# Optimization experiments

Measured on AMD Instinct MI355X. Metric: run time of the kernel, lower is better.

Reference implementation:

```python
import math
import jax, jax.numpy as jnp
import numpy as np

_GELU_C = math.sqrt(2.0 / math.pi)

def _gelu_tanh(x):
    return 0.5 * x * (1.0 + jnp.tanh(_GELU_C * (x + 0.044715 * x * x * x)))

def _l2_normalize(v, eps=1e-12):
    # matches F.normalize: v / max(||v||, eps)
    n = jnp.sqrt(jnp.sum(v * v, axis=-1, keepdims=True))
    return v / jnp.maximum(n, eps)

def setup_inputs() -> dict:
    key = jax.random.key(0)
    k1, k2, k3 = jax.random.split(key, 3)
    B, T, D = 8, 2048, 1024
    x = jax.random.normal(k1, (B, T, D), dtype=jnp.float32)
    # nn.Parameter initial values from the module
    log_alpha = jnp.asarray(math.log(math.exp(0.5) - 1.0), dtype=jnp.float32)
    log_sigma = jnp.asarray(math.log(1.0), dtype=jnp.float32)
    return {"x": x, "log_alpha": log_alpha, "log_sigma": log_sigma}

def reference(x, log_alpha, log_sigma):
    B, T, D = x.shape
    alpha = jax.nn.softplus(log_alpha)
    sigma = jax.nn.softplus(log_sigma)
    scale = 1.0 / math.sqrt(D)
    # full strictly-past causal attention (triu with diagonal=0 masks self too)
    sim = jnp.einsum('btd,bsd->bts', x, x) * scale            # [B,T,T]
    causal = jnp.triu(jnp.ones((T, T), dtype=bool), k=0)      # True = masked
    sim = jnp.where(causal[None], -jnp.inf, sim)
    # NaN-safe masked softmax: fully-masked rows (t=0) -> all zeros,
    # matching torch softmax + nan_to_num(nan=0.0)
    m = jnp.max(sim, axis=-1, keepdims=True)
    m_safe = jnp.where(jnp.isfinite(m), m, 0.0)
    e = jnp.exp(sim - m_safe)                                 # -inf -> 0
    denom = jnp.sum(e, axis=-1, keepdims=True)
    attn = jnp.where(denom > 0, e / jnp.where(denom > 0, denom, 1.0), 0.0)
    context = jnp.einsum('bts,bsd->btd', attn, x)             # [B,T,D]
    cos_sim = jnp.sum(_l2_normalize(x) * _l2_normalize(context), axis=-1)  # [B,T]
    novelty = jnp.clip(1.0 - cos_sim, 0.0, 2.0) / 2.0
    novelty = jnp.nan_to_num(novelty, nan=1.0)
    gate = 1.0 + alpha * jnp.tanh(sigma * novelty[..., None])
    return _gelu_tanh(x * gate)
```

## Files before the change

### kernel.cpp

```cpp
#include <hip/hip_runtime.h>
#include <math.h>

#define TN 2048
#define DN 1024
#define NEG_INF (-3.0e38f)

typedef __attribute__((ext_vector_type(8))) _Float16 half8;
typedef __attribute__((ext_vector_type(4))) _Float16 half4v;
typedef __attribute__((ext_vector_type(4))) float f32x4;

__device__ __forceinline__ f32x4 mfma16(half8 a, half8 b, f32x4 c) {
  return __builtin_amdgcn_mfma_f32_16x16x32_f16(a, b, c, 0, 0, 0);
}

#define BAR_LDS() asm volatile("s_waitcnt lgkmcnt(0)\ns_barrier" ::: "memory")

__device__ __forceinline__ int img_off(int key, int f) {
  const int kg = key >> 2;
  const int p  = ((kg & 1) << 2) | (kg >> 1);
  return (f >> 4) * 512 + p * 64 + (key & 3) * 16 + (f & 15);
}

__global__ __launch_bounds__(256) void convert_x(const float* __restrict__ x,
                                                 _Float16* __restrict__ w) {
  const long long gid = (long long)blockIdx.x * 256 + threadIdx.x;
  const long long e   = gid * 8;
  const int bt   = (int)(e >> 15);
  const int et   = (int)(e & 32767);
  const int f16b = et >> 9;
  const int p    = (et >> 6) & 7;
  const int row  = (et >> 4) & 3;
  const int col0 = et & 15;
  const int kg   = ((p & 3) << 1) | (p >> 2);
  const int key  = kg * 4 + row;
  const size_t xoff = ((size_t)bt * 32 + key) * DN + f16b * 16 + col0;
  float4 u0 = *(const float4*)(x + xoff);
  float4 u1 = *(const float4*)(x + xoff + 4);
  half8 h = {(_Float16)u0.x, (_Float16)u0.y, (_Float16)u0.z, (_Float16)u0.w,
             (_Float16)u1.x, (_Float16)u1.y, (_Float16)u1.z, (_Float16)u1.w};
  *(half8*)(w + e) = h;
}

template <bool WS>
__global__ __launch_bounds__(512)
void attn_gate(const float* __restrict__ x, const _Float16* __restrict__ wsx,
               const float* __restrict__ pla, const float* __restrict__ pls,
               float* __restrict__ out) {
  __shared__ _Float16 Kbuf[2][32768];
  __shared__ float Sred[4][32][34];
  __shared__ _Float16 Pq[32][40];
  __shared__ float m_s[32], l_s[32], corr_s[32], gate_s[32];

  const int tid = threadIdx.x;
  const int w   = tid >> 6;
  const int l   = tid & 63;
  const int lr  = l & 15;
  const int lg  = l >> 4;
  const int kq  = w & 3;
  const int ti  = w >> 2;

  const int b  = blockIdx.x & 7;
  const int pr = blockIdx.x >> 3;

  const float alpha = log1pf(expf(pla[0]));
  const float sigma = log1pf(expf(pls[0]));

  const float* xb = x + (size_t)b * TN * DN;
  float*       ob = out + (size_t)b * TN * DN;

  for (int hv = 0; hv < 2; ++hv) {
    const int qt    = hv ? (63 - pr) : pr;
    const int qbase = qt * 32;
    const int nkt   = qt + 1;

    if constexpr (WS) {
      const _Float16* t0 = wsx + (size_t)(b * 64 + 0) * 32768;
#pragma unroll
      for (int i = 0; i < 8; ++i)
        __builtin_amdgcn_global_load_lds(
            (const __attribute__((address_space(1))) void*)(t0 + w * 4096 + i * 512 + l * 8),
            (__attribute__((address_space(3))) void*)(&Kbuf[0][w * 4096 + i * 512]), 16, 0, 0);
      if (nkt > 1) {
        const _Float16* t1 = wsx + (size_t)(b * 64 + 1) * 32768;
#pragma unroll
        for (int i = 0; i < 8; ++i)
          __builtin_amdgcn_global_load_lds(
              (const __attribute__((address_space(1))) void*)(t1 + w * 4096 + i * 512 + l * 8),
              (__attribute__((address_space(3))) void*)(&Kbuf[1][w * 4096 + i * 512]), 16, 0, 0);
      }
    } else {
      const int skey = tid >> 4, sc = tid & 15;
      for (int t = 0; t < (nkt > 1 ? 2 : 1); ++t) {
        const float* kp = xb + (size_t)(t * 32 + skey) * DN + sc * 4;
#pragma unroll
        for (int j = 0; j < 16; ++j) {
          const int f = sc * 4 + 64 * j;
          float4 v = *(const float4*)(kp + 64 * j);
          half4v h = {(_Float16)v.x, (_Float16)v.y, (_Float16)v.z, (_Float16)v.w};
          *(half4v*)&Kbuf[t][img_off(skey, f)] = h;
        }
      }
    }

    half8 qf[8];
    if constexpr (WS) {
      const _Float16* qtile = wsx + (size_t)(b * 64 + qt) * 32768;
      const int qrow = ti * 16 + lr;
      const int qkg  = qrow >> 2;
      const int qp   = (((qkg & 1) << 2) | (qkg >> 1)) * 64 + (qrow & 3) * 16 + (lg & 1) * 8;
#pragma unroll
      for (int s = 0; s < 8; ++s)
        qf[s] = *(const half8*)&qtile[(kq * 16 + s * 2 + (lg >> 1)) * 512 + qp];
    } else {
      const float* qp = xb + (size_t)(qbase + ti * 16 + lr) * DN + kq * 256 + lg * 8;
#pragma unroll
      for (int s = 0; s < 8; ++s) {
        float4 a = ((const float4*)(qp + s * 32))[0];
        float4 c = ((const float4*)(qp + s * 32))[1];
        half8 h;
        h[0]=(_Float16)a.x; h[1]=(_Float16)a.y; h[2]=(_Float16)a.z; h[3]=(_Float16)a.w;
        h[4]=(_Float16)c.x; h[5]=(_Float16)c.y; h[6]=(_Float16)c.z; h[7]=(_Float16)c.w;
        qf[s] = h;
      }
    }

    f32x4 oacc[2][8];
#pragma unroll
    for (int rt = 0; rt < 2; ++rt)
#pragma unroll
      for (int ct = 0; ct < 8; ++ct)
        oacc[rt][ct] = f32x4{0.f, 0.f, 0.f, 0.f};

    if (tid < 32) { m_s[tid] = NEG_INF; l_s[tid] = 0.0f; }
    __syncthreads();

    const int kg0  = lr >> 2;
    const int bk0  = ((((kg0 & 1) << 2) | (kg0 >> 1)) << 6) + (lr & 3) * 16 + (lg & 1) * 8;
    const int kg1  = 4 + (lr >> 2);
    const int bk1  = ((((kg1 & 1) << 2) | (kg1 >> 1)) << 6) + (lr & 3) * 16 + (lg & 1) * 8;

    for (int kt = 0; kt < nkt; ++kt) {
      const int cur = kt & 1;

      {
        f32x4 s0 = f32x4{0.f, 0.f, 0.f, 0.f};
        f32x4 s1 = f32x4{0.f, 0.f, 0.f, 0.f};
        const _Float16* kb = &Kbuf[cur][0];
#pragma unroll
        for (int s = 0; s < 8; ++s) {
          const int base = (kq * 16 + s * 2 + (lg >> 1)) * 512;
          half8 bf0 = *(const half8*)&kb[base + bk0];
          half8 bf1 = *(const half8*)&kb[base + bk1];
          s0 = mfma16(qf[s], bf0, s0);
          s1 = mfma16(qf[s], bf1, s1);
        }
#pragma unroll
        for (int j = 0; j < 4; ++j) {
          Sred[kq][ti * 16 + lg * 4 + j][lr]      = s0[j];
          Sred[kq][ti * 16 + lg * 4 + j][16 + lr] = s1[j];
        }
      }
      BAR_LDS();

      {
        const int r   = tid >> 4;
        const int c0  = tid & 15;
        const int qg  = qbase + r;
        const int kb0 = kt * 32;
        float s0 = (Sred[0][r][c0] + Sred[1][r][c0] +
                    Sred[2][r][c0] + Sred[3][r][c0]) * 0.03125f;
        float s1 = (Sred[0][r][c0 + 16] + Sred[1][r][c0 + 16] +
                    Sred[2][r][c0 + 16] + Sred[3][r][c0 + 16]) * 0.03125f;
        const bool v0 = (kb0 + c0)      < qg;
        const bool v1 = (kb0 + c0 + 16) < qg;
        if (!v0) s0 = NEG_INF;
        if (!v1) s1 = NEG_INF;
        float tmax = fmaxf(s0, s1);
#pragma unroll
        for (int d = 1; d < 16; d <<= 1) tmax = fmaxf(tmax, __shfl_xor(tmax, d));
        const float m_old = m_s[r];
        const float m_new = fmaxf(m_old, tmax);
        float p0 = v0 ? __expf(s0 - m_new) : 0.0f;
        float p1 = v1 ? __expf(s1 - m_new) : 0.0f;
        float ps = p0 + p1;
#pragma unroll
        for (int d = 1; d < 16; d <<= 1) ps += __shfl_xor(ps, d);
        const float corr = (m_old > 0.5f * NEG_INF) ? __expf(m_old - m_new) : 0.0f;
        if (c0 == 0) {
          m_s[r]    = m_new;
          l_s[r]    = l_s[r] * corr + ps;
          corr_s[r] = corr;
        }
        Pq[r][c0]      = (_Float16)p0;
        Pq[r][c0 + 16] = (_Float16)p1;
      }
      BAR_LDS();

      {
#pragma unroll
        for (int rt = 0; rt < 2; ++rt)
#pragma unroll
          for (int j = 0; j < 4; ++j) {
            const float cr = corr_s[rt * 16 + lg * 4 + j];
#pragma unroll
            for (int ct = 0; ct < 8; ++ct) oacc[rt][ct][j] *= cr;
          }
        half8 a0 = *(const half8*)&Pq[lr][lg * 8];
        half8 a1 = *(const half8*)&Pq[16 + lr][lg * 8];
        half4v lo[8], hi[8];
        const uint32_t ab =
            (uint32_t)(uintptr_t)(void*)&Kbuf[cur][w * 4096 + l * 4];
#define TRRD(CT, O0, O1)                                                      \
        asm volatile("ds_read_b64_tr_b16 %0, %2 offset:" O0 "\n\t"            \
                     "ds_read_b64_tr_b16 %1, %2 offset:" O1                   \
                     : "=v"(lo[CT]), "=v"(hi[CT]) : "v"(ab));
        TRRD(0, "0",    "512")  TRRD(1, "1024", "1536")
        TRRD(2, "2048", "2560") TRRD(3, "3072", "3584")
        TRRD(4, "4096", "4608") TRRD(5, "5120", "5632")
        TRRD(6, "6144", "6656") TRRD(7, "7168", "7680")
#undef TRRD
        asm volatile("s_waitcnt lgkmcnt(0)" ::: "memory");
        __builtin_amdgcn_sched_barrier(0);
#pragma unroll
        for (int ct = 0; ct < 8; ++ct) {
          half8 bf = __builtin_shufflevector(lo[ct], hi[ct], 0, 1, 2, 3, 4, 5, 6, 7);
          oacc[0][ct] = mfma16(a0, bf, oacc[0][ct]);
          oacc[1][ct] = mfma16(a1, bf, oacc[1][ct]);
        }
      }
      __syncthreads();

      if (kt + 2 < nkt) {
        if constexpr (WS) {
          const _Float16* tn = wsx + (size_t)(b * 64 + kt + 2) * 32768;
#pragma unroll
          for (int i = 0; i < 8; ++i)
            __builtin_amdgcn_global_load_lds(
                (const __attribute__((address_space(1))) void*)(tn + w * 4096 + i * 512 + l * 8),
                (__attribute__((address_space(3))) void*)(&Kbuf[cur][w * 4096 + i * 512]), 16, 0, 0);
        } else {
          const int skey = tid >> 4, sc = tid & 15;
          const float* kp = xb + (size_t)((kt + 2) * 32 + skey) * DN + sc * 4;
#pragma unroll
          for (int j = 0; j < 16; ++j) {
            const int f = sc * 4 + 64 * j;
            float4 v = *(const float4*)(kp + 64 * j);
            half4v h = {(_Float16)v.x, (_Float16)v.y, (_Float16)v.z, (_Float16)v.w};
            *(half4v*)&Kbuf[cur][img_off(skey, f)] = h;
          }
        }
      }
    }

    {
      float* ered = &Sred[0][0][0];
#pragma unroll
      for (int rt = 0; rt < 2; ++rt)
#pragma unroll
        for (int j = 0; j < 4; ++j) {
          const int row = rt * 16 + lg * 4 + j;
          const float* xr = xb + (size_t)(qbase + row) * DN + w * 128 + lr;
          float a1 = 0.f, a2 = 0.f, a3 = 0.f;
#pragma unroll
          for (int ct = 0; ct < 8; ++ct) {
            const float xv = xr[ct * 16];
            const float ov = oacc[rt][ct][j];
            a1 += xv * ov; a2 += xv * xv; a3 += ov * ov;
          }
#pragma unroll
          for (int d = 1; d < 16; d <<= 1) {
            a1 += __shfl_xor(a1, d);
            a2 += __shfl_xor(a2, d);
            a3 += __shfl_xor(a3, d);
          }
          if (lr == 0) {
            float* e = ered + (row * 8 + w) * 4;
            e[0] = a1; e[1] = a2; e[2] = a3;
          }
        }
    }
    __syncthreads();
    if (tid < 32) {
      const float* ered = &Sred[0][0][0];
      float SxO = 0.f, Sxx = 0.f, SOO = 0.f;
#pragma unroll
      for (int wv = 0; wv < 8; ++wv) {
        const float* e = ered + (tid * 8 + wv) * 4;
        SxO += e[0]; Sxx += e[1]; SOO += e[2];
      }
      const float lden = l_s[tid];
      float cosv = 0.0f;
      if (lden > 0.0f) {
        const float nx = fmaxf(sqrtf(Sxx), 1e-12f);
        const float nc = fmaxf(sqrtf(SOO) / lden, 1e-12f);
        cosv = (SxO / lden) / (nx * nc);
      }
      float nov = fminf(fmaxf(1.0f - cosv, 0.0f), 2.0f) * 0.5f;
      gate_s[tid] = 1.0f + alpha * tanhf(sigma * nov);
    }
    __syncthreads();
    {
#pragma unroll
      for (int rt = 0; rt < 2; ++rt)
#pragma unroll
        for (int j = 0; j < 4; ++j) {
          const int row = rt * 16 + lg * 4 + j;
          const float g = gate_s[row];
          const float* xr = xb + (size_t)(qbase + row) * DN + w * 128 + lr;
          float* orow     = ob + (size_t)(qbase + row) * DN + w * 128 + lr;
#pragma unroll
          for (int ct = 0; ct < 8; ++ct) {
            const float z = xr[ct * 16] * g;
            const float u = 0.7978845608028654f * (z + 0.044715f * z * z * z);
            orow[ct * 16] = 0.5f * z * (1.0f + tanhf(u));
          }
        }
    }
    __syncthreads();
  }
}

extern "C" void kernel_launch(void* const* d_in, const int* in_sizes, int n_in,
                              void* d_out, int out_size, void* d_ws, size_t ws_size,
                              hipStream_t stream) {
  const float* x  = (const float*)d_in[0];
  const float* la = (const float*)d_in[1];
  const float* ls = (const float*)d_in[2];
  float* out = (float*)d_out;
  const size_t need = (size_t)8 * 64 * 32768 * 2;
  if (ws_size >= need) {
    convert_x<<<dim3(8192), dim3(256), 0, stream>>>(x, (_Float16*)d_ws);
    attn_gate<true><<<dim3(256), dim3(512), 0, stream>>>(
        x, (const _Float16*)d_ws, la, ls, out);
  } else {
    attn_gate<false><<<dim3(256), dim3(512), 0, stream>>>(
        x, (const _Float16*)nullptr, la, ls, out);
  }
}
```

Before: 196.5 us.

## Single-buffer K tile, one query tile per block, raise occupancy to 4 blocks/CU

Each block now handles one query tile (heaviest first) instead of a paired light/heavy tile, and the grid doubles to 512 blocks. The K tile drops from double to single buffering, and the score-reduction scratch is stored as fp16, shrinking LDS so that launch bounds of 4 blocks per CU can hold. The P·V step now interleaves transposed LDS reads with MFMAs and skips the accumulator rescale when no row max changed. The aim is latency hiding through more concurrent blocks rather than in-block prefetch, at the cost of an exposed load per key tile, less balanced per-block work, and fp16 rounding of partial scores.

```diff
diff --git a/kernel.cpp b/kernel.cpp
--- a/kernel.cpp
+++ b/kernel.cpp
@@ -7,13 +7,15 @@
 
 typedef __attribute__((ext_vector_type(8))) _Float16 half8;
 typedef __attribute__((ext_vector_type(4))) _Float16 half4v;
+typedef __attribute__((ext_vector_type(2))) _Float16 half2v;
 typedef __attribute__((ext_vector_type(4))) float f32x4;
 
 __device__ __forceinline__ f32x4 mfma16(half8 a, half8 b, f32x4 c) {
   return __builtin_amdgcn_mfma_f32_16x16x32_f16(a, b, c, 0, 0, 0);
 }
 
-#define BAR_LDS() asm volatile("s_waitcnt lgkmcnt(0)\ns_barrier" ::: "memory")
+#define BAR_LDS()  asm volatile("s_waitcnt lgkmcnt(0)\ns_barrier" ::: "memory")
+#define BAR_ALL()  asm volatile("s_waitcnt vmcnt(0) lgkmcnt(0)\ns_barrier" ::: "memory")
 
 __device__ __forceinline__ int img_off(int key, int f) {
   const int kg = key >> 2;
@@ -41,15 +43,34 @@
   *(half8*)(w + e) = h;
 }
 
+#define ISSUE4(T, O0, O1, O2, O3)                                             \
+  asm volatile("ds_read_b64_tr_b16 %0, %4 offset:" O0 "\n\t"                  \
+               "ds_read_b64_tr_b16 %1, %4 offset:" O1 "\n\t"                  \
+               "ds_read_b64_tr_b16 %2, %4 offset:" O2 "\n\t"                  \
+               "ds_read_b64_tr_b16 %3, %4 offset:" O3                         \
+               : "=&v"(T[0]), "=&v"(T[1]), "=&v"(T[2]), "=&v"(T[3])           \
+               : "v"(ab));
+
+#define MFMA4(T, CT0, CT1)                                                    \
+  {                                                                           \
+    half8 bf0 = __builtin_shufflevector(T[0], T[1], 0, 1, 2, 3, 4, 5, 6, 7);  \
+    half8 bf1 = __builtin_shufflevector(T[2], T[3], 0, 1, 2, 3, 4, 5, 6, 7);  \
+    oacc[0][CT0] = mfma16(a0, bf0, oacc[0][CT0]);                             \
+    oacc[1][CT0] = mfma16(a1, bf0, oacc[1][CT0]);                             \
+    oacc[0][CT1] = mfma16(a0, bf1, oacc[0][CT1]);                             \
+    oacc[1][CT1] = mfma16(a1, bf1, oacc[1][CT1]);                             \
+  }
+
 template <bool WS>
-__global__ __launch_bounds__(512)
+__global__ __launch_bounds__(512, 4)
 void attn_gate(const float* __restrict__ x, const _Float16* __restrict__ wsx,
                const float* __restrict__ pla, const float* __restrict__ pls,
                float* __restrict__ out) {
-  __shared__ _Float16 Kbuf[2][32768];
-  __shared__ float Sred[4][32][34];
+  __shared__ _Float16 Kbuf[32768];
+  __shared__ _Float16 SredH[4][32][17][2];
   __shared__ _Float16 Pq[32][40];
   __shared__ float m_s[32], l_s[32], corr_s[32], gate_s[32];
+  __shared__ int resc_s;
 
   const int tid = threadIdx.x;
   const int w   = tid >> 6;
@@ -60,7 +81,9 @@
   const int ti  = w >> 2;
 
   const int b  = blockIdx.x & 7;
-  const int pr = blockIdx.x >> 3;
+  const int qt = 63 - (blockIdx.x >> 3);
+  const int qbase = qt * 32;
+  const int nkt   = qt + 1;
 
   const float alpha = log1pf(expf(pla[0]));
   const float sigma = log1pf(expf(pls[0]));
@@ -68,255 +91,251 @@
   const float* xb = x + (size_t)b * TN * DN;
   float*       ob = out + (size_t)b * TN * DN;
 
-  for (int hv = 0; hv < 2; ++hv) {
-    const int qt    = hv ? (63 - pr) : pr;
-    const int qbase = qt * 32;
-    const int nkt   = qt + 1;
-
-    if constexpr (WS) {
-      const _Float16* t0 = wsx + (size_t)(b * 64 + 0) * 32768;
-#pragma unroll
-      for (int i = 0; i < 8; ++i)
-        __builtin_amdgcn_global_load_lds(
-            (const __attribute__((address_space(1))) void*)(t0 + w * 4096 + i * 512 + l * 8),
-            (__attribute__((address_space(3))) void*)(&Kbuf[0][w * 4096 + i * 512]), 16, 0, 0);
-      if (nkt > 1) {
-        const _Float16* t1 = wsx + (size_t)(b * 64 + 1) * 32768;
+  if constexpr (WS) {
+    const _Float16* t0 = wsx + (size_t)(b * 64 + 0) * 32768;
+#pragma unroll
+    for (int i = 0; i < 8; ++i)
+      __builtin_amdgcn_global_load_lds(
+          (const __attribute__((address_space(1))) void*)(t0 + w * 4096 + i * 512 + l * 8),
+          (__attribute__((address_space(3))) void*)(&Kbuf[w * 4096 + i * 512]), 16, 0, 0);
+  } else {
+    const int skey = tid >> 4, sc = tid & 15;
+    const float* kp = xb + (size_t)skey * DN + sc * 4;
+#pragma unroll
+    for (int j = 0; j < 16; ++j) {
+      const int f = sc * 4 + 64 * j;
+      float4 v = *(const float4*)(kp + 64 * j);
+      half4v h = {(_Float16)v.x, (_Float16)v.y, (_Float16)v.z, (_Float16)v.w};
+      *(half4v*)&Kbuf[img_off(skey, f)] = h;
+    }
+  }
+
+  half8 qf[8];
+  if constexpr (WS) {
+    const _Float16* qtile = wsx + (size_t)(b * 64 + qt) * 32768;
+    const int qrow = ti * 16 + lr;
+    const int qkg  = qrow >> 2;
+    const int qp   = (((qkg & 1) << 2) | (qkg >> 1)) * 64 + (qrow & 3) * 16 + (lg & 1) * 8;
+#pragma unroll
+    for (int s = 0; s < 8; ++s)
+      qf[s] = *(const half8*)&qtile[(kq * 16 + s * 2 + (lg >> 1)) * 512 + qp];
+  } else {
+    const float* qp = xb + (size_t)(qbase + ti * 16 + lr) * DN + kq * 256 + lg * 8;
+#pragma unroll
+    for (int s = 0; s < 8; ++s) {
+      float4 a = ((const float4*)(qp + s * 32))[0];
+      float4 c = ((const float4*)(qp + s * 32))[1];
+      half8 h;
+      h[0]=(_Float16)a.x; h[1]=(_Float16)a.y; h[2]=(_Float16)a.z; h[3]=(_Float16)a.w;
+      h[4]=(_Float16)c.x; h[5]=(_Float16)c.y; h[6]=(_Float16)c.z; h[7]=(_Float16)c.w;
+      qf[s] = h;
+    }
+  }
+
+  f32x4 oacc[2][8];
+#pragma unroll
+  for (int rt = 0; rt < 2; ++rt)
+#pragma unroll
+    for (int ct = 0; ct < 8; ++ct)
+      oacc[rt][ct] = f32x4{0.f, 0.f, 0.f, 0.f};
+
+  if (tid < 32) { m_s[tid] = NEG_INF; l_s[tid] = 0.0f; }
+  if (tid == 0) resc_s = 0;
+  BAR_ALL();
+
+  const int kg0 = lr >> 2;
+  const int bk0 = ((((kg0 & 1) << 2) | (kg0 >> 1)) << 6) + (lr & 3) * 16 + (lg & 1) * 8;
+  const int kg1 = 4 + (lr >> 2);
+  const int bk1 = ((((kg1 & 1) << 2) | (kg1 >> 1)) << 6) + (lr & 3) * 16 + (lg & 1) * 8;
+
+  for (int kt = 0; kt < nkt; ++kt) {
+    if (tid == 0) resc_s = 0;
+
+    {
+      f32x4 s0 = f32x4{0.f, 0.f, 0.f, 0.f};
+      f32x4 s1 = f32x4{0.f, 0.f, 0.f, 0.f};
+#pragma unroll
+      for (int s = 0; s < 8; ++s) {
+        const int base = (kq * 16 + s * 2 + (lg >> 1)) * 512;
+        half8 bf0 = *(const half8*)&Kbuf[base + bk0];
+        half8 bf1 = *(const half8*)&Kbuf[base + bk1];
+        s0 = mfma16(qf[s], bf0, s0);
+        s1 = mfma16(qf[s], bf1, s1);
+      }
+#pragma unroll
+      for (int j = 0; j < 4; ++j) {
+        half2v pr2 = {(_Float16)s0[j], (_Float16)s1[j]};
+        *(half2v*)&SredH[kq][ti * 16 + lg * 4 + j][lr][0] = pr2;
+      }
+    }
+    BAR_LDS();
+
+    {
+      const int r   = tid >> 4;
+      const int c0  = tid & 15;
+      const int qg  = qbase + r;
+      const int kb0 = kt * 32;
+      float s0 = 0.f, s1 = 0.f;
+#pragma unroll
+      for (int k4 = 0; k4 < 4; ++k4) {
+        half2v v = *(const half2v*)&SredH[k4][r][c0][0];
+        s0 += (float)v[0];
+        s1 += (float)v[1];
+      }
+      s0 *= 0.03125f; s1 *= 0.03125f;
+      const bool v0 = (kb0 + c0)      < qg;
+      const bool v1 = (kb0 + c0 + 16) < qg;
+      if (!v0) s0 = NEG_INF;
+      if (!v1) s1 = NEG_INF;
+      float tmax = fmaxf(s0, s1);
+#pragma unroll
+      for (int d = 1; d < 16; d <<= 1) tmax = fmaxf(tmax, __shfl_xor(tmax, d));
+      const float m_old = m_s[r];
+      const float m_new = fmaxf(m_old, tmax);
+      float p0 = v0 ? __expf(s0 - m_new) : 0.0f;
+      float p1 = v1 ? __expf(s1 - m_new) : 0.0f;
+      float ps = p0 + p1;
+#pragma unroll
+      for (int d = 1; d < 16; d <<= 1) ps += __shfl_xor(ps, d);
+      if (c0 == 0) {
+        const float corr = (m_old > 0.5f * NEG_INF) ? __expf(m_old - m_new) : 0.0f;
+        m_s[r]    = m_new;
+        l_s[r]    = l_s[r] * corr + ps;
+        corr_s[r] = corr;
+        if (m_new > m_old) resc_s = 1;
+      }
+      Pq[r][c0]      = (_Float16)p0;
+      Pq[r][c0 + 16] = (_Float16)p1;
+    }
+    BAR_LDS();
+
+    {
+      const int doresc = resc_s;
+      if (doresc) {
+#pragma unroll
+        for (int rt = 0; rt < 2; ++rt)
+#pragma unroll
+          for (int j = 0; j < 4; ++j) {
+            const float cr2 = corr_s[rt * 16 + lg * 4 + j];
+#pragma unroll
+            for (int ct = 0; ct < 8; ++ct) oacc[rt][ct][j] *= cr2;
+          }
+      }
+      const uint32_t pa0 = (uint32_t)(uintptr_t)(void*)&Pq[lr][lg * 8];
+      const uint32_t pa1 = (uint32_t)(uintptr_t)(void*)&Pq[16 + lr][lg * 8];
+      const uint32_t ab  = (uint32_t)(uintptr_t)(void*)&Kbuf[w * 4096 + l * 4];
+      asm volatile("s_waitcnt lgkmcnt(0)" ::: "memory");
+      __builtin_amdgcn_sched_barrier(0);
+      half8 a0, a1;
+      half4v t0[4], t1[4];
+      asm volatile("ds_read_b128 %0, %2\n\t"
+                   "ds_read_b128 %1, %3"
+                   : "=&v"(a0), "=&v"(a1) : "v"(pa0), "v"(pa1));
+      ISSUE4(t0, "0", "512", "1024", "1536");
+      ISSUE4(t1, "2048", "2560", "3072", "3584");
+      asm volatile("s_waitcnt lgkmcnt(4)" ::: "memory");
+      __builtin_amdgcn_sched_barrier(0);
+      MFMA4(t0, 0, 1);
+      ISSUE4(t0, "4096", "4608", "5120", "5632");
+      asm volatile("s_waitcnt lgkmcnt(4)" ::: "memory");
+      __builtin_amdgcn_sched_barrier(0);
+      MFMA4(t1, 2, 3);
+      ISSUE4(t1, "6144", "6656", "7168", "7680");
+      asm volatile("s_waitcnt lgkmcnt(4)" ::: "memory");
+      __builtin_amdgcn_sched_barrier(0);
+      MFMA4(t0, 4, 5);
+      asm volatile("s_waitcnt lgkmcnt(0)" ::: "memory");
+      __builtin_amdgcn_sched_barrier(0);
+      MFMA4(t1, 6, 7);
+    }
+    BAR_LDS();
+
+    if (kt + 1 < nkt) {
+      if constexpr (WS) {
+        const _Float16* tn = wsx + (size_t)(b * 64 + kt + 1) * 32768;
 #pragma unroll
         for (int i = 0; i < 8; ++i)
           __builtin_amdgcn_global_load_lds(
-              (const __attribute__((address_space(1))) void*)(t1 + w * 4096 + i * 512 + l * 8),
-              (__attribute__((address_space(3))) void*)(&Kbuf[1][w * 4096 + i * 512]), 16, 0, 0);
-      }
-    } else {
-      const int skey = tid >> 4, sc = tid & 15;
-      for (int t = 0; t < (nkt > 1 ? 2 : 1); ++t) {
-        const float* kp = xb + (size_t)(t * 32 + skey) * DN + sc * 4;
+              (const __attribute__((address_space(1))) void*)(tn + w * 4096 + i * 512 + l * 8),
+              (__attribute__((address_space(3))) void*)(&Kbuf[w * 4096 + i * 512]), 16, 0, 0);
+      } else {
+        const int skey = tid >> 4, sc = tid & 15;
+        const float* kp = xb + (size_t)((kt + 1) * 32 + skey) * DN + sc * 4;
 #pragma unroll
         for (int j = 0; j < 16; ++j) {
           const int f = sc * 4 + 64 * j;
           float4 v = *(const float4*)(kp + 64 * j);
           half4v h = {(_Float16)v.x, (_Float16)v.y, (_Float16)v.z, (_Float16)v.w};
-          *(half4v*)&Kbuf[t][img_off(skey, f)] = h;
-        }
-      }
-    }
-
-    half8 qf[8];
-    if constexpr (WS) {
-      const _Float16* qtile = wsx + (size_t)(b * 64 + qt) * 32768;
-      const int qrow = ti * 16 + lr;
-      const int qkg  = qrow >> 2;
-      const int qp   = (((qkg & 1) << 2) | (qkg >> 1)) * 64 + (qrow & 3) * 16 + (lg & 1) * 8;
-#pragma unroll
-      for (int s = 0; s < 8; ++s)
-        qf[s] = *(const half8*)&qtile[(kq * 16 + s * 2 + (lg >> 1)) * 512 + qp];
-    } else {
-      const float* qp = xb + (size_t)(qbase + ti * 16 + lr) * DN + kq * 256 + lg * 8;
-#pragma unroll
-      for (int s = 0; s < 8; ++s) {
-        float4 a = ((const float4*)(qp + s * 32))[0];
-        float4 c = ((const float4*)(qp + s * 32))[1];
-        half8 h;
-        h[0]=(_Float16)a.x; h[1]=(_Float16)a.y; h[2]=(_Float16)a.z; h[3]=(_Float16)a.w;
-        h[4]=(_Float16)c.x; h[5]=(_Float16)c.y; h[6]=(_Float16)c.z; h[7]=(_Float16)c.w;
-        qf[s] = h;
-      }
-    }
-
-    f32x4 oacc[2][8];
+          *(half4v*)&Kbuf[img_off(skey, f)] = h;
+        }
+      }
+      BAR_ALL();
+    }
+  }
+
+  {
+    float* ered = (float*)&SredH[0][0][0][0];
 #pragma unroll
     for (int rt = 0; rt < 2; ++rt)
 #pragma unroll
-      for (int ct = 0; ct < 8; ++ct)
-        oacc[rt][ct] = f32x4{0.f, 0.f, 0.f, 0.f};
-
-    if (tid < 32) { m_s[tid] = NEG_INF; l_s[tid] = 0.0f; }
-    __syncthreads();
-
-    const int kg0  = lr >> 2;
-    const int bk0  = ((((kg0 & 1) << 2) | (kg0 >> 1)) << 6) + (lr & 3) * 16 + (lg & 1) * 8;
-    const int kg1  = 4 + (lr >> 2);
-    const int bk1  = ((((kg1 & 1) << 2) | (kg1 >> 1)) << 6) + (lr & 3) * 16 + (lg & 1) * 8;
-
-    for (int kt = 0; kt < nkt; ++kt) {
-      const int cur = kt & 1;
-
-      {
-        f32x4 s0 = f32x4{0.f, 0.f, 0.f, 0.f};
-        f32x4 s1 = f32x4{0.f, 0.f, 0.f, 0.f};
-        const _Float16* kb = &Kbuf[cur][0];
-#pragma unroll
-        for (int s = 0; s < 8; ++s) {
-          const int base = (kq * 16 + s * 2 + (lg >> 1)) * 512;
-          half8 bf0 = *(const half8*)&kb[base + bk0];
-          half8 bf1 = *(const half8*)&kb[base + bk1];
-          s0 = mfma16(qf[s], bf0, s0);
-          s1 = mfma16(qf[s], bf1, s1);
-        }
-#pragma unroll
-        for (int j = 0; j < 4; ++j) {
-          Sred[kq][ti * 16 + lg * 4 + j][lr]      = s0[j];
-          Sred[kq][ti * 16 + lg * 4 + j][16 + lr] = s1[j];
-        }
-      }
-      BAR_LDS();
-
-      {
-        const int r   = tid >> 4;
-        const int c0  = tid & 15;
-        const int qg  = qbase + r;
-        const int kb0 = kt * 32;
-        float s0 = (Sred[0][r][c0] + Sred[1][r][c0] +
-                    Sred[2][r][c0] + Sred[3][r][c0]) * 0.03125f;
-        float s1 = (Sred[0][r][c0 + 16] + Sred[1][r][c0 + 16] +
-                    Sred[2][r][c0 + 16] + Sred[3][r][c0 + 16]) * 0.03125f;
-        const bool v0 = (kb0 + c0)      < qg;
-        const bool v1 = (kb0 + c0 + 16) < qg;
-        if (!v0) s0 = NEG_INF;
-        if (!v1) s1 = NEG_INF;
-        float tmax = fmaxf(s0, s1);
-#pragma unroll
-        for (int d = 1; d < 16; d <<= 1) tmax = fmaxf(tmax, __shfl_xor(tmax, d));
-        const float m_old = m_s[r];
-        const float m_new = fmaxf(m_old, tmax);
-        float p0 = v0 ? __expf(s0 - m_new) : 0.0f;
-        float p1 = v1 ? __expf(s1 - m_new) : 0.0f;
-        float ps = p0 + p1;
-#pragma unroll
-        for (int d = 1; d < 16; d <<= 1) ps += __shfl_xor(ps, d);
-        const float corr = (m_old > 0.5f * NEG_INF) ? __expf(m_old - m_new) : 0.0f;
-        if (c0 == 0) {
-          m_s[r]    = m_new;
-          l_s[r]    = l_s[r] * corr + ps;
-          corr_s[r] = corr;
-        }
-        Pq[r][c0]      = (_Float16)p0;
-        Pq[r][c0 + 16] = (_Float16)p1;
-      }
-      BAR_LDS();
-
-      {
-#pragma unroll
-        for (int rt = 0; rt < 2; ++rt)
-#pragma unroll
-          for (int j = 0; j < 4; ++j) {
-            const float cr = corr_s[rt * 16 + lg * 4 + j];
-#pragma unroll
-            for (int ct = 0; ct < 8; ++ct) oacc[rt][ct][j] *= cr;
-          }
-        half8 a0 = *(const half8*)&Pq[lr][lg * 8];
-        half8 a1 = *(const half8*)&Pq[16 + lr][lg * 8];
-        half4v lo[8], hi[8];
-        const uint32_t ab =
-            (uint32_t)(uintptr_t)(void*)&Kbuf[cur][w * 4096 + l * 4];
-#define TRRD(CT, O0, O1)                                                      \
-        asm volatile("ds_read_b64_tr_b16 %0, %2 offset:" O0 "\n\t"            \
-                     "ds_read_b64_tr_b16 %1, %2 offset:" O1                   \
-                     : "=v"(lo[CT]), "=v"(hi[CT]) : "v"(ab));
-        TRRD(0, "0",    "512")  TRRD(1, "1024", "1536")
-        TRRD(2, "2048", "2560") TRRD(3, "3072", "3584")
-        TRRD(4, "4096", "4608") TRRD(5, "5120", "5632")
-        TRRD(6, "6144", "6656") TRRD(7, "7168", "7680")
-#undef TRRD
-        asm volatile("s_waitcnt lgkmcnt(0)" ::: "memory");
-        __builtin_amdgcn_sched_barrier(0);
+      for (int j = 0; j < 4; ++j) {
+        const int row = rt * 16 + lg * 4 + j;
+        const float* xr = xb + (size_t)(qbase + row) * DN + w * 128 + lr;
+        float a1 = 0.f, a2 = 0.f, a3 = 0.f;
 #pragma unroll
         for (int ct = 0; ct < 8; ++ct) {
-          half8 bf = __builtin_shufflevector(lo[ct], hi[ct], 0, 1, 2, 3, 4, 5, 6, 7);
-          oacc[0][ct] = mfma16(a0, bf, oacc[0][ct]);
-          oacc[1][ct] = mfma16(a1, bf, oacc[1][ct]);
-        }
-      }
-      __syncthreads();
-
-      if (kt + 2 < nkt) {
-        if constexpr (WS) {
-          const _Float16* tn = wsx + (size_t)(b * 64 + kt + 2) * 32768;
-#pragma unroll
-          for (int i = 0; i < 8; ++i)
-            __builtin_amdgcn_global_load_lds(
-                (const __attribute__((address_space(1))) void*)(tn + w * 4096 + i * 512 + l * 8),
-                (__attribute__((address_space(3))) void*)(&Kbuf[cur][w * 4096 + i * 512]), 16, 0, 0);
-        } else {
-          const int skey = tid >> 4, sc = tid & 15;
-          const float* kp = xb + (size_t)((kt + 2) * 32 + skey) * DN + sc * 4;
-#pragma unroll
-          for (int j = 0; j < 16; ++j) {
-            const int f = sc * 4 + 64 * j;
-            float4 v = *(const float4*)(kp + 64 * j);
-            half4v h = {(_Float16)v.x, (_Float16)v.y, (_Float16)v.z, (_Float16)v.w};
-            *(half4v*)&Kbuf[cur][img_off(skey, f)] = h;
-          }
-        }
-      }
-    }
-
-    {
-      float* ered = &Sred[0][0][0];
-#pragma unroll
-      for (int rt = 0; rt < 2; ++rt)
-#pragma unroll
-        for (int j = 0; j < 4; ++j) {
-          const int row = rt * 16 + lg * 4 + j;
-          const float* xr = xb + (size_t)(qbase + row) * DN + w * 128 + lr;
-          float a1 = 0.f, a2 = 0.f, a3 = 0.f;
-#pragma unroll
-          for (int ct = 0; ct < 8; ++ct) {
-            const float xv = xr[ct * 16];
-            const float ov = oacc[rt][ct][j];
-            a1 += xv * ov; a2 += xv * xv; a3 += ov * ov;
-          }
-#pragma unroll
-          for (int d = 1; d < 16; d <<= 1) {
-            a1 += __shfl_xor(a1, d);
-            a2 += __shfl_xor(a2, d);
-            a3 += __shfl_xor(a3, d);
-          }
-          if (lr == 0) {
-            float* e = ered + (row * 8 + w) * 4;
-            e[0] = a1; e[1] = a2; e[2] = a3;
-          }
-        }
-    }
-    __syncthreads();
-    if (tid < 32) {
-      const float* ered = &Sred[0][0][0];
-      float SxO = 0.f, Sxx = 0.f, SOO = 0.f;
-#pragma unroll
-      for (int wv = 0; wv < 8; ++wv) {
-        const float* e = ered + (tid * 8 + wv) * 4;
-        SxO += e[0]; Sxx += e[1]; SOO += e[2];
-      }
-      const float lden = l_s[tid];
-      float cosv = 0.0f;
-      if (lden > 0.0f) {
-        const float nx = fmaxf(sqrtf(Sxx), 1e-12f);
-        const float nc = fmaxf(sqrtf(SOO) / lden, 1e-12f);
-        cosv = (SxO / lden) / (nx * nc);
-      }
-      float nov = fminf(fmaxf(1.0f - cosv, 0.0f), 2.0f) * 0.5f;
-      gate_s[tid] = 1.0f + alpha * tanhf(sigma * nov);
-    }
-    __syncthreads();
-    {
-#pragma unroll
-      for (int rt = 0; rt < 2; ++rt)
-#pragma unroll
-        for (int j = 0; j < 4; ++j) {
-          const int row = rt * 16 + lg * 4 + j;
-          const float g = gate_s[row];
-          const float* xr = xb + (size_t)(qbase + row) * DN + w * 128 + lr;
-          float* orow     = ob + (size_t)(qbase + row) * DN + w * 128 + lr;
-#pragma unroll
-          for (int ct = 0; ct < 8; ++ct) {
-            const float z = xr[ct * 16] * g;
-            const float u = 0.7978845608028654f * (z + 0.044715f * z * z * z);
-            orow[ct * 16] = 0.5f * z * (1.0f + tanhf(u));
-          }
-        }
-    }
-    __syncthreads();
+          const float xv = xr[ct * 16];
+          const float ov = oacc[rt][ct][j];
+          a1 += xv * ov; a2 += xv * xv; a3 += ov * ov;
+        }
+#pragma unroll
+        for (int d = 1; d < 16; d <<= 1) {
+          a1 += __shfl_xor(a1, d);
+          a2 += __shfl_xor(a2, d);
+          a3 += __shfl_xor(a3, d);
+        }
+        if (lr == 0) {
+          float* e = ered + (row * 8 + w) * 4;
+          e[0] = a1; e[1] = a2; e[2] = a3;
+        }
+      }
+  }
+  __syncthreads();
+  if (tid < 32) {
+    const float* ered = (const float*)&SredH[0][0][0][0];
+    float SxO = 0.f, Sxx = 0.f, SOO = 0.f;
+#pragma unroll
+    for (int wv = 0; wv < 8; ++wv) {
+      const float* e = ered + (tid * 8 + wv) * 4;
+      SxO += e[0]; Sxx += e[1]; SOO += e[2];
+    }
+    const float lden = l_s[tid];
+    float cosv = 0.0f;
+    if (lden > 0.0f) {
+      const float nx = fmaxf(sqrtf(Sxx), 1e-12f);
+      const float nc = fmaxf(sqrtf(SOO) / lden, 1e-12f);
+      cosv = (SxO / lden) / (nx * nc);
+    }
+    float nov = fminf(fmaxf(1.0f - cosv, 0.0f), 2.0f) * 0.5f;
+    gate_s[tid] = 1.0f + alpha * tanhf(sigma * nov);
+  }
+  __syncthreads();
+  {
+#pragma unroll
+    for (int rt = 0; rt < 2; ++rt)
+#pragma unroll
+      for (int j = 0; j < 4; ++j) {
+        const int row = rt * 16 + lg * 4 + j;
+        const float g = gate_s[row];
+        const float* xr = xb + (size_t)(qbase + row) * DN + w * 128 + lr;
+        float* orow     = ob + (size_t)(qbase + row) * DN + w * 128 + lr;
+#pragma unroll
+        for (int ct = 0; ct < 8; ++ct) {
+          const float z = xr[ct * 16] * g;
+          const float u = 0.7978845608028654f * (z + 0.044715f * z * z * z);
+          orow[ct * 16] = 0.5f * z * (1.0f + tanhf(u));
+        }
+      }
   }
 }
 
@@ -330,10 +349,10 @@
   const size_t need = (size_t)8 * 64 * 32768 * 2;
   if (ws_size >= need) {
     convert_x<<<dim3(8192), dim3(256), 0, stream>>>(x, (_Float16*)d_ws);
-    attn_gate<true><<<dim3(256), dim3(512), 0, stream>>>(
+    attn_gate<true><<<dim3(512), dim3(512), 0, stream>>>(
         x, (const _Float16*)d_ws, la, ls, out);
   } else {
-    attn_gate<false><<<dim3(256), dim3(512), 0, stream>>>(
+    attn_gate<false><<<dim3(512), dim3(512), 0, stream>>>(
         x, (const _Float16*)nullptr, la, ls, out);
   }
 }
```

Measured after the change: 299.8 us. 52.6% more time.
